# Performance work log

Measured on AMD Instinct MI355X. Metric: run time of the kernel, lower is better.

The kernel has to match this reference:

```python
import jax, jax.numpy as jnp
import numpy as np
from jax import lax

B, H, L, N, COUT = 16, 128, 8192, 16, 128
NEG_SLOPE = 0.3
BN_EPS = 1e-5


def setup_inputs() -> dict:
    key = jax.random.key(0)
    ks = jax.random.split(key, 20)
    x = jax.random.normal(ks[0], (B, H, L), dtype=jnp.float32)
    # --- S4D parameters ---
    log_dt = jnp.log(0.001) + jax.random.uniform(ks[1], (H,), dtype=jnp.float32) * (jnp.log(0.1) - jnp.log(0.001))
    A_log = jnp.log(0.5 * jnp.ones((H, N), dtype=jnp.float32))  # real part magnitude
    A_imag = jnp.broadcast_to(np.pi * jnp.arange(N, dtype=jnp.float32), (H, N)).copy()
    B_re = jnp.ones((H, N), dtype=jnp.float32)
    B_im = jnp.zeros((H, N), dtype=jnp.float32)
    C_re = jax.random.normal(ks[2], (H, N), dtype=jnp.float32) * (0.5 ** 0.5)
    C_im = jax.random.normal(ks[3], (H, N), dtype=jnp.float32) * (0.5 ** 0.5)
    D = jax.random.normal(ks[4], (H,), dtype=jnp.float32)
    # --- dilated conv branches (kernel_size=3, stride=4) ---
    wscale = 1.0 / np.sqrt(H * 3)
    w1 = jax.random.normal(ks[5], (COUT, H, 3), dtype=jnp.float32) * wscale
    b1 = jnp.zeros((COUT,), dtype=jnp.float32)
    w2 = jax.random.normal(ks[6], (COUT, H, 3), dtype=jnp.float32) * wscale
    b2 = jnp.zeros((COUT,), dtype=jnp.float32)
    w3 = jax.random.normal(ks[7], (COUT, H, 3), dtype=jnp.float32) * wscale
    b3 = jnp.zeros((COUT,), dtype=jnp.float32)
    w4 = jax.random.normal(ks[8], (COUT, H, 3), dtype=jnp.float32) * wscale
    b4 = jnp.zeros((COUT,), dtype=jnp.float32)
    gamma = jnp.ones((COUT,), dtype=jnp.float32)
    beta = jnp.zeros((COUT,), dtype=jnp.float32)
    return dict(x=x, log_dt=log_dt, A_log=A_log, A_imag=A_imag, B_re=B_re, B_im=B_im,
                C_re=C_re, C_im=C_im, D=D, w1=w1, b1=b1, w2=w2, b2=b2, w3=w3, b3=b3,
                w4=w4, b4=b4, gamma=gamma, beta=beta)


def _s4d(x, log_dt, A_log, A_imag, B_re, B_im, C_re, C_im, D):
    # x: (B,H,L). S4D with ZOH discretization, FFT long convolution.
    Lx = x.shape[-1]
    dt = jnp.exp(log_dt)[:, None]                    # (H,1)
    A = -jnp.exp(A_log) + 1j * A_imag                # (H,N)
    dtA = dt * A                                     # (H,N)
    dB = (jnp.exp(dtA) - 1.0) / A * (B_re + 1j * B_im)
    CB = (C_re + 1j * C_im) * dB                     # (H,N)
    l = jnp.arange(Lx, dtype=jnp.float32)
    vand = jnp.exp(dtA[:, :, None] * l)              # (H,N,L) Vandermonde
    K = 2.0 * jnp.real(jnp.einsum('hn,hnl->hl', CB, vand))  # (H,L)
    n = 2 * Lx
    Uf = jnp.fft.rfft(x, n=n)                        # (B,H,L+1)
    Kf = jnp.fft.rfft(K, n=n)                        # (H,L+1)
    y = jnp.fft.irfft(Uf * Kf, n=n)[..., :Lx]
    return y + D[:, None] * x


def _dconv(x, w, b, dil, pad):
    y = lax.conv_general_dilated(x, w, window_strides=(4,), padding=[(pad, pad)],
                                 rhs_dilation=(dil,), dimension_numbers=('NCH', 'OIH', 'NCH'))
    return y + b[:, None]


def _bn(z, gamma, beta):
    # training-mode BatchNorm1d: batch stats over (B, L_out) per channel
    m = jnp.mean(z, axis=(0, 2), keepdims=True)
    v = jnp.var(z, axis=(0, 2), keepdims=True)
    return gamma[:, None] * (z - m) * lax.rsqrt(v + BN_EPS) + beta[:, None]


def _lrelu(z):
    return jnp.where(z >= 0, z, NEG_SLOPE * z)


def reference(x, log_dt, A_log, A_imag, B_re, B_im, C_re, C_im, D,
              w1, b1, w2, b2, w3, b3, w4, b4, gamma, beta):
    y = _s4d(x, log_dt, A_log, A_imag, B_re, B_im, C_re, C_im, D)
    d1 = _bn(_dconv(y, w1, b1, 1, 1), gamma, beta)                 # no activation on branch 1
    d2 = _bn(_lrelu(_dconv(y, w2, b2, 2, 2)), gamma, beta)
    d3 = _bn(_lrelu(_dconv(y, w3, b3, 4, 4)), gamma, beta)
    d4 = _bn(_lrelu(_dconv(y, w4, b4, 8, 8)), gamma, beta)
    return jnp.concatenate([d1, d2, d3, d4], axis=1)               # (B, 4*COUT, L//4)
```

## Files before the change

kernel.cpp:

```cpp
#include <hip/hip_runtime.h>
#include <math.h>

typedef unsigned short u16x8 __attribute__((ext_vector_type(8)));
typedef unsigned short u16x2 __attribute__((ext_vector_type(2)));
typedef short s16x8 __attribute__((ext_vector_type(8)));
typedef float f32x4 __attribute__((ext_vector_type(4)));

__device__ __forceinline__ float bf2f(unsigned short u) {
    union { unsigned int i; float f; } v; v.i = ((unsigned int)u) << 16; return v.f;
}
__device__ __forceinline__ unsigned short f2bf(float f) {
    union { unsigned int i; float f; } v; v.f = f;
    unsigned int r = v.i + 0x7FFFu + ((v.i >> 16) & 1u);
    return (unsigned short)(r >> 16);
}

#define WB_OFF   163840
#define STAT_OFF 557056
#define Y_OFF    1048576
#define YT_OFF   34603008
#define Z_OFF    Y_OFF

__global__ void precompute_params(const float* __restrict__ log_dt,
                                  const float* __restrict__ A_log,
                                  const float* __restrict__ A_imag,
                                  const float* __restrict__ B_re,
                                  const float* __restrict__ B_im,
                                  const float* __restrict__ C_re,
                                  const float* __restrict__ C_im,
                                  float* __restrict__ params)
{
    int i = blockIdx.x * 256 + threadIdx.x;
    if (i >= 2048) return;
    int h = i >> 4;
    double dt = exp((double)log_dt[h]);
    double Ar = -exp((double)A_log[i]);
    double Ai = (double)A_imag[i];
    double dr = dt * Ar, di = dt * Ai;
    double ew = exp(dr);
    double wr = ew * cos(di), wi = ew * sin(di);
    double nr = wr - 1.0, ni = wi;
    double inv = 1.0 / (Ar * Ar + Ai * Ai);
    double tr = (nr * Ar + ni * Ai) * inv;
    double ti = (ni * Ar - nr * Ai) * inv;
    double Br = (double)B_re[i], Bi = (double)B_im[i];
    double dbr = tr * Br - ti * Bi, dbi = tr * Bi + ti * Br;
    double Cr = (double)C_re[i], Ci = (double)C_im[i];
    double cbr = Cr * dbr - Ci * dbi, cbi = Cr * dbi + Ci * dbr;
    params[i]        = (float)wr;
    params[2048 + i] = (float)wi;
    params[4096 + i] = (float)(2.0 * cbr);
    params[6144 + i] = (float)(2.0 * cbi);
    #pragma unroll
    for (int k = 0; k < 8; k++) {
        double mm = (double)(32 << k);
        double er = exp(mm * dr);
        params[8192 + k * 4096 + i]        = (float)(er * cos(mm * di));
        params[8192 + k * 4096 + 2048 + i] = (float)(er * sin(mm * di));
    }
}

__global__ void wpack(const float* __restrict__ w1, const float* __restrict__ w2,
                      const float* __restrict__ w3, const float* __restrict__ w4,
                      unsigned short* __restrict__ WB)
{
    int idx = blockIdx.x * 256 + threadIdx.x;
    int br = idx / 49152;
    int r  = idx - br * 49152;
    int co = r / 384;
    int k  = r - co * 384;
    int tap = k >> 7, h = k & 127;
    const float* wp = (br == 0) ? w1 : (br == 1) ? w2 : (br == 2) ? w3 : w4;
    WB[idx] = f2bf(wp[co * 384 + h * 3 + tap]);
}

__global__ __launch_bounds__(256, 2) void s4d_scan(const float* __restrict__ x,
                                                   const float* __restrict__ params,
                                                   const float* __restrict__ Dp,
                                                   unsigned short* __restrict__ yout)
{
    __shared__ float sbuf[256 * 33];
    __shared__ float spow[256];
    const int tid = threadIdx.x;
    const int bh = blockIdx.x;
    const int h = bh & 127;

    {
        int k = tid >> 5, r = tid & 31, n = r >> 1, c = r & 1;
        spow[tid] = params[8192 + k * 4096 + c * 2048 + (h << 4) + n];
    }

    float wre[16], wim[16];
    #pragma unroll
    for (int n = 0; n < 16; n++) {
        wre[n] = params[(h << 4) + n];
        wim[n] = params[2048 + (h << 4) + n];
    }

    const float4* xp4 = (const float4*)(x + (((size_t)bh) << 13) + (tid << 5));

    float zr[16], zi[16];
    #pragma unroll
    for (int n = 0; n < 16; n++) { zr[n] = 0.f; zi[n] = 0.f; }

    for (int s4v = 0; s4v < 8; s4v++) {
        float4 xv4 = xp4[s4v];
        #pragma unroll
        for (int e = 0; e < 4; e++) {
            float xv = (e == 0) ? xv4.x : (e == 1) ? xv4.y : (e == 2) ? xv4.z : xv4.w;
            #pragma unroll
            for (int n = 0; n < 16; n++) {
                float nr = fmaf(wre[n], zr[n], fmaf(-wim[n], zi[n], xv));
                float ni = fmaf(wim[n], zr[n], wre[n] * zi[n]);
                zr[n] = nr; zi[n] = ni;
            }
        }
    }
    __syncthreads();

    #pragma unroll 1
    for (int k = 0; k < 8; k++) {
        const int o = 1 << k;
        #pragma unroll
        for (int n = 0; n < 16; n++) {
            sbuf[tid * 33 + 2 * n]     = zr[n];
            sbuf[tid * 33 + 2 * n + 1] = zi[n];
        }
        __syncthreads();
        if (tid >= o) {
            const float* lp = &sbuf[(tid - o) * 33];
            #pragma unroll
            for (int n = 0; n < 16; n++) {
                float lr = lp[2 * n], li = lp[2 * n + 1];
                float mr = spow[(k << 5) + 2 * n], mi = spow[(k << 5) + 2 * n + 1];
                zr[n] = fmaf(mr, lr, fmaf(-mi, li, zr[n]));
                zi[n] = fmaf(mr, li, fmaf(mi, lr, zi[n]));
            }
        }
        __syncthreads();
    }

    #pragma unroll
    for (int n = 0; n < 16; n++) {
        sbuf[tid * 33 + 2 * n]     = zr[n];
        sbuf[tid * 33 + 2 * n + 1] = zi[n];
    }
    __syncthreads();
    if (tid == 0) {
        #pragma unroll
        for (int n = 0; n < 16; n++) { zr[n] = 0.f; zi[n] = 0.f; }
    } else {
        const float* lp = &sbuf[(tid - 1) * 33];
        #pragma unroll
        for (int n = 0; n < 16; n++) { zr[n] = lp[2 * n]; zi[n] = lp[2 * n + 1]; }
    }

    float cbr[16], cbi[16];
    #pragma unroll
    for (int n = 0; n < 16; n++) {
        cbr[n] = params[4096 + (h << 4) + n];
        cbi[n] = params[6144 + (h << 4) + n];
    }
    const float Dh = Dp[h];
    u16x8* yp8 = (u16x8*)(yout + (((size_t)bh) << 13) + (tid << 5));

    for (int s8 = 0; s8 < 4; s8++) {
        float4 xa = xp4[2 * s8], xb = xp4[2 * s8 + 1];
        u16x8 pk;
        #pragma unroll
        for (int e = 0; e < 8; e++) {
            float xv;
            switch (e) {
                case 0: xv = xa.x; break; case 1: xv = xa.y; break;
                case 2: xv = xa.z; break; case 3: xv = xa.w; break;
                case 4: xv = xb.x; break; case 5: xv = xb.y; break;
                case 6: xv = xb.z; break; default: xv = xb.w; break;
            }
            float acc = Dh * xv;
            #pragma unroll
            for (int n = 0; n < 16; n++) {
                float nr = fmaf(wre[n], zr[n], fmaf(-wim[n], zi[n], xv));
                float ni = fmaf(wim[n], zr[n], wre[n] * zi[n]);
                zr[n] = nr; zi[n] = ni;
                acc = fmaf(cbr[n], nr, fmaf(-cbi[n], ni, acc));
            }
            pk[e] = f2bf(acc);
        }
        yp8[s8] = pk;
    }
}

__global__ __launch_bounds__(256) void ytrans(const unsigned short* __restrict__ y,
                                              unsigned short* __restrict__ yT)
{
    __shared__ unsigned short sT[128 * 72];
    const int b = blockIdx.y, g0 = blockIdx.x << 6;
    const int tid = threadIdx.x;
    #pragma unroll
    for (int j = 0; j < 4; j++) {
        int li = tid + (j << 8);
        int h = li >> 3, g8 = (li & 7) << 3;
        u16x8 v = *(const u16x8*)(y + (((size_t)(b * 128 + h)) << 13) + g0 + g8);
        int gp = (g8 + (((h >> 3) & 7) << 3)) & 63;
        *(u16x8*)&sT[h * 72 + gp] = v;
    }
    __syncthreads();
    #pragma unroll
    for (int j = 0; j < 4; j++) {
        int li = tid + (j << 8);
        int g = li >> 4, h8 = (li & 15) << 3;
        u16x8 o;
        #pragma unroll
        for (int e = 0; e < 8; e++) {
            int h = h8 + e;
            int gp = (g + (((h >> 3) & 7) << 3)) & 63;
            o[e] = sT[h * 72 + gp];
        }
        *(u16x8*)(yT + (((size_t)(b * 8192 + g0 + g)) << 7) + h8) = o;
    }
}

__global__ __launch_bounds__(256) void conv_mfma(
    const unsigned short* __restrict__ yT,
    const unsigned short* __restrict__ WB,
    const float* __restrict__ b1, const float* __restrict__ b2,
    const float* __restrict__ b3, const float* __restrict__ b4,
    unsigned short* __restrict__ z)
{
    __shared__ unsigned short sW[128 * 40];
    __shared__ unsigned short sY[128 * 40];
    const int tid = threadIdx.x;
    const int lane = tid & 63, w = tid >> 6;
    const int branch = blockIdx.z, b = blockIdx.y;
    const int t0 = blockIdx.x << 7;
    const int d = 1 << branch;
    const int coH = (w & 1) << 6, tH = (w >> 1) << 6;
    const int ml = lane & 15, kg = lane >> 4;

    f32x4 acc[4][4];
    #pragma unroll
    for (int mt = 0; mt < 4; mt++)
        #pragma unroll
        for (int nt = 0; nt < 4; nt++) acc[mt][nt] = (f32x4)(0.f);

    const unsigned short* WBb = WB + (size_t)branch * 49152;

    for (int kc = 0; kc < 12; kc++) {
        const int tap = kc >> 2, hc = (kc & 3) << 5;
        const int goff = d * (tap - 1);
        __syncthreads();
        #pragma unroll
        for (int j = 0; j < 2; j++) {
            int li = tid + (j << 8);
            int co = li >> 2, kq = (li & 3) << 3;
            u16x8 v = *(const u16x8*)(WBb + (size_t)co * 384 + (kc << 5) + kq);
            *(u16x8*)&sW[co * 40 + kq] = v;
        }
        #pragma unroll
        for (int j = 0; j < 2; j++) {
            int li = tid + (j << 8);
            int n = li >> 2, kq = (li & 3) << 3;
            int g = ((t0 + n) << 2) + goff;
            u16x8 v;
            if ((unsigned)g < 8192u) {
                v = *(const u16x8*)(yT + (((size_t)(b * 8192 + g)) << 7) + hc + kq);
            } else {
                #pragma unroll
                for (int e = 0; e < 8; e++) v[e] = 0;
            }
            *(u16x8*)&sY[n * 40 + kq] = v;
        }
        __syncthreads();
        s16x8 af[4], bf[4];
        #pragma unroll
        for (int mt = 0; mt < 4; mt++)
            af[mt] = *(const s16x8*)&sW[(coH + mt * 16 + ml) * 40 + (kg << 3)];
        #pragma unroll
        for (int nt = 0; nt < 4; nt++)
            bf[nt] = *(const s16x8*)&sY[(tH + nt * 16 + ml) * 40 + (kg << 3)];
        #pragma unroll
        for (int mt = 0; mt < 4; mt++)
            #pragma unroll
            for (int nt = 0; nt < 4; nt++)
                acc[mt][nt] = __builtin_amdgcn_mfma_f32_16x16x32_bf16(af[mt], bf[nt], acc[mt][nt], 0, 0, 0);
    }

    const float* bp = (branch == 0) ? b1 : (branch == 1) ? b2 : (branch == 2) ? b3 : b4;
    #pragma unroll
    for (int mt = 0; mt < 4; mt++) {
        #pragma unroll
        for (int r = 0; r < 4; r++) {
            const int co = coH + mt * 16 + (kg << 2) + r;
            const float bb = bp[co];
            #pragma unroll
            for (int nt = 0; nt < 4; nt++) {
                const int t = t0 + tH + nt * 16 + ml;
                float v = acc[mt][nt][r] + bb;
                if (branch != 0) v = (v >= 0.f) ? v : 0.3f * v;
                z[(((size_t)((branch * 16 + b) * 128 + co)) << 11) + t] = f2bf(v);
            }
        }
    }
}

__global__ __launch_bounds__(256) void bn_stats(const unsigned short* __restrict__ z,
                                                float* __restrict__ stats)
{
    const int bc = blockIdx.x;
    const int branch = bc >> 7, co = bc & 127;
    const int tid = threadIdx.x;
    float s1 = 0.f, s2 = 0.f;
    for (int i = tid; i < 16384; i += 256) {
        int b = i >> 10, tp = (i & 1023) << 1;
        const unsigned short* p = z + (((size_t)((branch * 16 + b) * 128 + co)) << 11) + tp;
        u16x2 v2 = *(const u16x2*)p;
        float a = bf2f(v2[0]), c = bf2f(v2[1]);
        s1 += a + c;
        s2 = fmaf(a, a, fmaf(c, c, s2));
    }
    #pragma unroll
    for (int o = 32; o > 0; o >>= 1) { s1 += __shfl_down(s1, o); s2 += __shfl_down(s2, o); }
    __shared__ float r1[4], r2[4];
    const int lane = tid & 63, wid = tid >> 6;
    if (lane == 0) { r1[wid] = s1; r2[wid] = s2; }
    __syncthreads();
    if (tid == 0) {
        float t1 = r1[0] + r1[1] + r1[2] + r1[3];
        float t2 = r2[0] + r2[1] + r2[2] + r2[3];
        float m = t1 * (1.0f / 32768.0f);
        float var = t2 * (1.0f / 32768.0f) - m * m;
        stats[bc * 2]     = m;
        stats[bc * 2 + 1] = 1.0f / sqrtf(var + 1e-5f);
    }
}

__global__ __launch_bounds__(256) void bn_apply(const unsigned short* __restrict__ z,
                                                const float* __restrict__ stats,
                                                const float* __restrict__ gam,
                                                const float* __restrict__ bet,
                                                float* __restrict__ out)
{
    const size_t idx = (((size_t)blockIdx.x << 8) + threadIdx.x) << 3;
    const int t = (int)(idx & 2047);
    const size_t bc = idx >> 11;
    const int ch = (int)(bc & 511);
    const int b = (int)(bc >> 9);
    const int branch = ch >> 7, co = ch & 127;
    const float m = stats[ch * 2], inv = stats[ch * 2 + 1];
    const float ga = gam[co], be = bet[co];
    const float sc = ga * inv, sh = fmaf(-m, sc, be);
    const unsigned short* zp = z + (((size_t)((branch * 16 + b) * 128 + co)) << 11) + t;
    u16x8 v = *(const u16x8*)zp;
    float4 o0, o1;
    o0.x = fmaf(bf2f(v[0]), sc, sh); o0.y = fmaf(bf2f(v[1]), sc, sh);
    o0.z = fmaf(bf2f(v[2]), sc, sh); o0.w = fmaf(bf2f(v[3]), sc, sh);
    o1.x = fmaf(bf2f(v[4]), sc, sh); o1.y = fmaf(bf2f(v[5]), sc, sh);
    o1.z = fmaf(bf2f(v[6]), sc, sh); o1.w = fmaf(bf2f(v[7]), sc, sh);
    *(float4*)(out + idx)     = o0;
    *(float4*)(out + idx + 4) = o1;
}

extern "C" void kernel_launch(void* const* d_in, const int* in_sizes, int n_in,
                              void* d_out, int out_size, void* d_ws, size_t ws_size,
                              hipStream_t stream) {
    const float* x      = (const float*)d_in[0];
    const float* log_dt = (const float*)d_in[1];
    const float* A_log  = (const float*)d_in[2];
    const float* A_imag = (const float*)d_in[3];
    const float* B_re   = (const float*)d_in[4];
    const float* B_im   = (const float*)d_in[5];
    const float* C_re   = (const float*)d_in[6];
    const float* C_im   = (const float*)d_in[7];
    const float* Dp     = (const float*)d_in[8];
    const float* w1 = (const float*)d_in[9];
    const float* b1 = (const float*)d_in[10];
    const float* w2 = (const float*)d_in[11];
    const float* b2 = (const float*)d_in[12];
    const float* w3 = (const float*)d_in[13];
    const float* b3 = (const float*)d_in[14];
    const float* w4 = (const float*)d_in[15];
    const float* b4 = (const float*)d_in[16];
    const float* gam = (const float*)d_in[17];
    const float* bet = (const float*)d_in[18];

    float* params = (float*)d_ws;
    unsigned short* WBp = (unsigned short*)((char*)d_ws + WB_OFF);
    float* stats = (float*)((char*)d_ws + STAT_OFF);
    unsigned short* yws = (unsigned short*)((char*)d_ws + Y_OFF);
    unsigned short* yT  = (unsigned short*)((char*)d_ws + YT_OFF);
    unsigned short* zws = (unsigned short*)((char*)d_ws + Z_OFF);
    float* out = (float*)d_out;

    precompute_params<<<dim3(8), dim3(256), 0, stream>>>(log_dt, A_log, A_imag,
                                                         B_re, B_im, C_re, C_im, params);
    wpack<<<dim3(768), dim3(256), 0, stream>>>(w1, w2, w3, w4, WBp);
    s4d_scan<<<dim3(2048), dim3(256), 0, stream>>>(x, params, Dp, yws);
    ytrans<<<dim3(128, 16), dim3(256), 0, stream>>>(yws, yT);
    conv_mfma<<<dim3(16, 16, 4), dim3(256), 0, stream>>>(yT, WBp, b1, b2, b3, b4, zws);
    bn_stats<<<dim3(512), dim3(256), 0, stream>>>(zws, stats);
    bn_apply<<<dim3(8192), dim3(256), 0, stream>>>(zws, stats, gam, bet, out);
}
```

Measured before the change: 294.9 us.

## Replace sequential S4D chunk recurrence with bf16 MFMA chunked state-space matmuls

After: 284.1 us. 3.7% less time.

```diff
diff --git a/kernel.cpp b/kernel.cpp
--- a/kernel.cpp
+++ b/kernel.cpp
@@ -15,48 +15,96 @@
     return (unsigned short)(r >> 16);
 }
 
-#define WB_OFF   163840
-#define STAT_OFF 557056
+#define MATS_OFF 16384
+#define WB_OFF   548864
+#define STAT_OFF 942080
 #define Y_OFF    1048576
 #define YT_OFF   34603008
 #define Z_OFF    Y_OFF
 
-__global__ void precompute_params(const float* __restrict__ log_dt,
-                                  const float* __restrict__ A_log,
-                                  const float* __restrict__ A_imag,
-                                  const float* __restrict__ B_re,
-                                  const float* __restrict__ B_im,
-                                  const float* __restrict__ C_re,
-                                  const float* __restrict__ C_im,
-                                  float* __restrict__ params)
-{
-    int i = blockIdx.x * 256 + threadIdx.x;
-    if (i >= 2048) return;
-    int h = i >> 4;
-    double dt = exp((double)log_dt[h]);
-    double Ar = -exp((double)A_log[i]);
-    double Ai = (double)A_imag[i];
-    double dr = dt * Ar, di = dt * Ai;
-    double ew = exp(dr);
-    double wr = ew * cos(di), wi = ew * sin(di);
-    double nr = wr - 1.0, ni = wi;
-    double inv = 1.0 / (Ar * Ar + Ai * Ai);
-    double tr = (nr * Ar + ni * Ai) * inv;
-    double ti = (ni * Ar - nr * Ai) * inv;
-    double Br = (double)B_re[i], Bi = (double)B_im[i];
-    double dbr = tr * Br - ti * Bi, dbi = tr * Bi + ti * Br;
-    double Cr = (double)C_re[i], Ci = (double)C_im[i];
-    double cbr = Cr * dbr - Ci * dbi, cbi = Cr * dbi + Ci * dbr;
-    params[i]        = (float)wr;
-    params[2048 + i] = (float)wi;
-    params[4096 + i] = (float)(2.0 * cbr);
-    params[6144 + i] = (float)(2.0 * cbi);
-    #pragma unroll
-    for (int k = 0; k < 8; k++) {
-        double mm = (double)(32 << k);
-        double er = exp(mm * dr);
-        params[8192 + k * 4096 + i]        = (float)(er * cos(mm * di));
-        params[8192 + k * 4096 + 2048 + i] = (float)(er * sin(mm * di));
+__global__ void precompute_s4d(const float* __restrict__ log_dt,
+                               const float* __restrict__ A_log,
+                               const float* __restrict__ A_imag,
+                               const float* __restrict__ B_re,
+                               const float* __restrict__ B_im,
+                               const float* __restrict__ C_re,
+                               const float* __restrict__ C_im,
+                               float* __restrict__ w32,
+                               unsigned short* __restrict__ MATS)
+{
+    const int h = blockIdx.x;
+    const int tid = threadIdx.x;
+    const double dt = exp((double)log_dt[h]);
+
+    #pragma unroll 1
+    for (int it = 0; it < 4; it++) {
+        int idx = tid + (it << 8);
+        int s = idx >> 5, i = idx & 31;
+        int n = s >> 1;
+        double Ar = -exp((double)A_log[h * 16 + n]);
+        double Ai = (double)A_imag[h * 16 + n];
+        double dr = dt * Ar, di = dt * Ai;
+        double l = (double)(31 - i);
+        double e = exp(l * dr);
+        double val = (s & 1) ? e * sin(l * di) : e * cos(l * di);
+        MATS[(size_t)h * 2080 + s * 32 + i] = f2bf((float)val);
+    }
+    #pragma unroll 1
+    for (int it = 0; it < 4; it++) {
+        int idx = tid + (it << 8);
+        int j = idx >> 5, s = idx & 31;
+        int n = s >> 1;
+        double Ar = -exp((double)A_log[h * 16 + n]);
+        double Ai = (double)A_imag[h * 16 + n];
+        double dr = dt * Ar, di = dt * Ai;
+        double ew = exp(dr);
+        double wr = ew * cos(di), wi = ew * sin(di);
+        double nr = wr - 1.0, ni = wi;
+        double inv = 1.0 / (Ar * Ar + Ai * Ai);
+        double tr = (nr * Ar + ni * Ai) * inv;
+        double ti = (ni * Ar - nr * Ai) * inv;
+        double Br = (double)B_re[h * 16 + n], Bi = (double)B_im[h * 16 + n];
+        double dbr = tr * Br - ti * Bi, dbi = tr * Bi + ti * Br;
+        double Cr = (double)C_re[h * 16 + n], Ci = (double)C_im[h * 16 + n];
+        double cbr = Cr * dbr - Ci * dbi, cbi = Cr * dbi + Ci * dbr;
+        double m = (double)(j + 1);
+        double e = exp(m * dr);
+        double pr = e * cos(m * di), pi = e * sin(m * di);
+        double gr = cbr * pr - cbi * pi, gi = cbr * pi + cbi * pr;
+        double val = (s & 1) ? -2.0 * gi : 2.0 * gr;
+        MATS[(size_t)h * 2080 + 1024 + j * 32 + s] = f2bf((float)val);
+    }
+    if (tid < 32) {
+        double l = (double)tid;
+        double acc = 0.0;
+        for (int n = 0; n < 16; n++) {
+            double Ar = -exp((double)A_log[h * 16 + n]);
+            double Ai = (double)A_imag[h * 16 + n];
+            double dr = dt * Ar, di = dt * Ai;
+            double ew = exp(dr);
+            double wr = ew * cos(di), wi = ew * sin(di);
+            double nr = wr - 1.0, ni = wi;
+            double inv = 1.0 / (Ar * Ar + Ai * Ai);
+            double tr = (nr * Ar + ni * Ai) * inv;
+            double ti = (ni * Ar - nr * Ai) * inv;
+            double Br = (double)B_re[h * 16 + n], Bi = (double)B_im[h * 16 + n];
+            double dbr = tr * Br - ti * Bi, dbi = tr * Bi + ti * Br;
+            double Cr = (double)C_re[h * 16 + n], Ci = (double)C_im[h * 16 + n];
+            double cbr = Cr * dbr - Ci * dbi, cbi = Cr * dbi + Ci * dbr;
+            double e = exp(l * dr);
+            double wlr = e * cos(l * di), wli = e * sin(l * di);
+            acc += cbr * wlr - cbi * wli;
+        }
+        MATS[(size_t)h * 2080 + 2048 + tid] = f2bf((float)(2.0 * acc));
+    }
+    if (tid < 16) {
+        int n = tid;
+        double Ar = -exp((double)A_log[h * 16 + n]);
+        double Ai = (double)A_imag[h * 16 + n];
+        double dr = dt * Ar, di = dt * Ai;
+        double e = exp(32.0 * dr);
+        w32[h * 32 + 2 * n]     = (float)(e * cos(32.0 * di));
+        w32[h * 32 + 2 * n + 1] = (float)(e * sin(32.0 * di));
     }
 }
 
@@ -74,47 +122,96 @@
     WB[idx] = f2bf(wp[co * 384 + h * 3 + tap]);
 }
 
-__global__ __launch_bounds__(256, 2) void s4d_scan(const float* __restrict__ x,
-                                                   const float* __restrict__ params,
+__global__ __launch_bounds__(256, 2) void s4d_mfma(const float* __restrict__ x,
+                                                   const float* __restrict__ w32,
+                                                   const unsigned short* __restrict__ MATS,
                                                    const float* __restrict__ Dp,
                                                    unsigned short* __restrict__ yout)
 {
-    __shared__ float sbuf[256 * 33];
-    __shared__ float spow[256];
+    __shared__ unsigned short sXc[256 * 40];
+    __shared__ unsigned short sM[3840];
+    __shared__ float spow2[256];
+    __shared__ unsigned short skr[32];
+    __shared__ float scratch[8448];
     const int tid = threadIdx.x;
     const int bh = blockIdx.x;
     const int h = bh & 127;
-
+    const int lane = tid & 63, w = tid >> 6;
+    const int ml = lane & 15, kg = lane >> 4;
+
+    float xr[32];
+    const float4* xp4 = (const float4*)(x + ((size_t)bh << 13) + (tid << 5));
+    #pragma unroll
+    for (int i = 0; i < 8; i++) {
+        float4 v = xp4[i];
+        xr[4 * i] = v.x; xr[4 * i + 1] = v.y; xr[4 * i + 2] = v.z; xr[4 * i + 3] = v.w;
+    }
+    #pragma unroll
+    for (int g = 0; g < 4; g++) {
+        u16x8 pk;
+        #pragma unroll
+        for (int e = 0; e < 8; e++) pk[e] = f2bf(xr[g * 8 + e]);
+        *(u16x8*)&sXc[tid * 40 + g * 8] = pk;
+    }
     {
-        int k = tid >> 5, r = tid & 31, n = r >> 1, c = r & 1;
-        spow[tid] = params[8192 + k * 4096 + c * 2048 + (h << 4) + n];
-    }
-
-    float wre[16], wim[16];
+        int matv = tid >> 7, r = (tid >> 2) & 31, sg = tid & 3;
+        u16x8 v = *(const u16x8*)(MATS + (size_t)h * 2080 + matv * 1024 + r * 32 + sg * 8);
+        *(u16x8*)&sM[matv * 2560 + r * 40 + sg * 8] = v;
+    }
+    if (tid < 4) {
+        u16x8 v = *(const u16x8*)(MATS + (size_t)h * 2080 + 2048 + tid * 8);
+        *(u16x8*)&skr[tid * 8] = v;
+    }
+    if (tid < 16) {
+        float rr = w32[h * 32 + 2 * tid], ii = w32[h * 32 + 2 * tid + 1];
+        #pragma unroll
+        for (int k = 0; k < 8; k++) {
+            spow2[k * 32 + 2 * tid] = rr; spow2[k * 32 + 2 * tid + 1] = ii;
+            float n2r = rr * rr - ii * ii, n2i = 2.f * rr * ii;
+            rr = n2r; ii = n2i;
+        }
+    }
+    __syncthreads();
+    #pragma unroll
+    for (int it = 0; it < 4; it++) {
+        int idx = tid + (it << 8);
+        int j = idx >> 5, i = idx & 31;
+        sM[1280 + j * 40 + i] = (i <= j) ? skr[j - i] : (unsigned short)0;
+    }
+    __syncthreads();
+
+    f32x4 acc[2][4];
+    #pragma unroll
+    for (int mt = 0; mt < 2; mt++)
+        #pragma unroll
+        for (int nt = 0; nt < 4; nt++) acc[mt][nt] = (f32x4)(0.f);
+    {
+        s16x8 af[2], bfr[4];
+        #pragma unroll
+        for (int mt = 0; mt < 2; mt++)
+            af[mt] = *(const s16x8*)&sM[(mt * 16 + ml) * 40 + kg * 8];
+        #pragma unroll
+        for (int nt = 0; nt < 4; nt++)
+            bfr[nt] = *(const s16x8*)&sXc[(w * 64 + nt * 16 + ml) * 40 + kg * 8];
+        #pragma unroll
+        for (int mt = 0; mt < 2; mt++)
+            #pragma unroll
+            for (int nt = 0; nt < 4; nt++)
+                acc[mt][nt] = __builtin_amdgcn_mfma_f32_16x16x32_bf16(af[mt], bfr[nt], acc[mt][nt], 0, 0, 0);
+    }
+    #pragma unroll
+    for (int mt = 0; mt < 2; mt++)
+        #pragma unroll
+        for (int nt = 0; nt < 4; nt++)
+            #pragma unroll
+            for (int r = 0; r < 4; r++)
+                scratch[(mt * 16 + kg * 4 + r) * 264 + (w * 64 + nt * 16 + ml)] = acc[mt][nt][r];
+    __syncthreads();
+    float zr[16], zi[16];
     #pragma unroll
     for (int n = 0; n < 16; n++) {
-        wre[n] = params[(h << 4) + n];
-        wim[n] = params[2048 + (h << 4) + n];
-    }
-
-    const float4* xp4 = (const float4*)(x + (((size_t)bh) << 13) + (tid << 5));
-
-    float zr[16], zi[16];
-    #pragma unroll
-    for (int n = 0; n < 16; n++) { zr[n] = 0.f; zi[n] = 0.f; }
-
-    for (int s4v = 0; s4v < 8; s4v++) {
-        float4 xv4 = xp4[s4v];
-        #pragma unroll
-        for (int e = 0; e < 4; e++) {
-            float xv = (e == 0) ? xv4.x : (e == 1) ? xv4.y : (e == 2) ? xv4.z : xv4.w;
-            #pragma unroll
-            for (int n = 0; n < 16; n++) {
-                float nr = fmaf(wre[n], zr[n], fmaf(-wim[n], zi[n], xv));
-                float ni = fmaf(wim[n], zr[n], wre[n] * zi[n]);
-                zr[n] = nr; zi[n] = ni;
-            }
-        }
+        zr[n] = scratch[(2 * n) * 264 + tid];
+        zi[n] = scratch[(2 * n + 1) * 264 + tid];
     }
     __syncthreads();
 
@@ -123,70 +220,97 @@
         const int o = 1 << k;
         #pragma unroll
         for (int n = 0; n < 16; n++) {
-            sbuf[tid * 33 + 2 * n]     = zr[n];
-            sbuf[tid * 33 + 2 * n + 1] = zi[n];
+            scratch[tid * 33 + 2 * n]     = zr[n];
+            scratch[tid * 33 + 2 * n + 1] = zi[n];
         }
         __syncthreads();
         if (tid >= o) {
-            const float* lp = &sbuf[(tid - o) * 33];
+            const float* lp = &scratch[(tid - o) * 33];
             #pragma unroll
             for (int n = 0; n < 16; n++) {
                 float lr = lp[2 * n], li = lp[2 * n + 1];
-                float mr = spow[(k << 5) + 2 * n], mi = spow[(k << 5) + 2 * n + 1];
+                float mr = spow2[(k << 5) + 2 * n], mi = spow2[(k << 5) + 2 * n + 1];
                 zr[n] = fmaf(mr, lr, fmaf(-mi, li, zr[n]));
                 zi[n] = fmaf(mr, li, fmaf(mi, lr, zi[n]));
             }
         }
         __syncthreads();
     }
-
     #pragma unroll
     for (int n = 0; n < 16; n++) {
-        sbuf[tid * 33 + 2 * n]     = zr[n];
-        sbuf[tid * 33 + 2 * n + 1] = zi[n];
+        scratch[tid * 33 + 2 * n]     = zr[n];
+        scratch[tid * 33 + 2 * n + 1] = zi[n];
     }
     __syncthreads();
     if (tid == 0) {
         #pragma unroll
         for (int n = 0; n < 16; n++) { zr[n] = 0.f; zi[n] = 0.f; }
     } else {
-        const float* lp = &sbuf[(tid - 1) * 33];
+        const float* lp = &scratch[(tid - 1) * 33];
         #pragma unroll
         for (int n = 0; n < 16; n++) { zr[n] = lp[2 * n]; zi[n] = lp[2 * n + 1]; }
     }
-
-    float cbr[16], cbi[16];
-    #pragma unroll
-    for (int n = 0; n < 16; n++) {
-        cbr[n] = params[4096 + (h << 4) + n];
-        cbi[n] = params[6144 + (h << 4) + n];
-    }
+    __syncthreads();
+    {
+        unsigned short* sCc = (unsigned short*)scratch;
+        #pragma unroll
+        for (int g = 0; g < 4; g++) {
+            u16x8 pk;
+            #pragma unroll
+            for (int q = 0; q < 4; q++) {
+                pk[2 * q]     = f2bf(zr[g * 4 + q]);
+                pk[2 * q + 1] = f2bf(zi[g * 4 + q]);
+            }
+            *(u16x8*)&sCc[tid * 40 + g * 8] = pk;
+        }
+    }
+    __syncthreads();
+
+    #pragma unroll
+    for (int mt = 0; mt < 2; mt++)
+        #pragma unroll
+        for (int nt = 0; nt < 4; nt++) acc[mt][nt] = (f32x4)(0.f);
+    {
+        const unsigned short* sCc = (const unsigned short*)scratch;
+        s16x8 a1[2], a2[2], bfx[4], bfc[4];
+        #pragma unroll
+        for (int mt = 0; mt < 2; mt++) {
+            a1[mt] = *(const s16x8*)&sM[1280 + (mt * 16 + ml) * 40 + kg * 8];
+            a2[mt] = *(const s16x8*)&sM[2560 + (mt * 16 + ml) * 40 + kg * 8];
+        }
+        #pragma unroll
+        for (int nt = 0; nt < 4; nt++) {
+            bfx[nt] = *(const s16x8*)&sXc[(w * 64 + nt * 16 + ml) * 40 + kg * 8];
+            bfc[nt] = *(const s16x8*)&sCc[(w * 64 + nt * 16 + ml) * 40 + kg * 8];
+        }
+        #pragma unroll
+        for (int mt = 0; mt < 2; mt++)
+            #pragma unroll
+            for (int nt = 0; nt < 4; nt++) {
+                acc[mt][nt] = __builtin_amdgcn_mfma_f32_16x16x32_bf16(a1[mt], bfx[nt], acc[mt][nt], 0, 0, 0);
+                acc[mt][nt] = __builtin_amdgcn_mfma_f32_16x16x32_bf16(a2[mt], bfc[nt], acc[mt][nt], 0, 0, 0);
+            }
+    }
+    __syncthreads();
+    #pragma unroll
+    for (int mt = 0; mt < 2; mt++)
+        #pragma unroll
+        for (int nt = 0; nt < 4; nt++)
+            #pragma unroll
+            for (int r = 0; r < 4; r++)
+                scratch[(mt * 16 + kg * 4 + r) * 264 + (w * 64 + nt * 16 + ml)] = acc[mt][nt][r];
+    __syncthreads();
     const float Dh = Dp[h];
-    u16x8* yp8 = (u16x8*)(yout + (((size_t)bh) << 13) + (tid << 5));
-
-    for (int s8 = 0; s8 < 4; s8++) {
-        float4 xa = xp4[2 * s8], xb = xp4[2 * s8 + 1];
+    u16x8* yp = (u16x8*)(yout + ((size_t)bh << 13) + (tid << 5));
+    #pragma unroll
+    for (int g = 0; g < 4; g++) {
         u16x8 pk;
         #pragma unroll
         for (int e = 0; e < 8; e++) {
-            float xv;
-            switch (e) {
-                case 0: xv = xa.x; break; case 1: xv = xa.y; break;
-                case 2: xv = xa.z; break; case 3: xv = xa.w; break;
-                case 4: xv = xb.x; break; case 5: xv = xb.y; break;
-                case 6: xv = xb.z; break; default: xv = xb.w; break;
-            }
-            float acc = Dh * xv;
-            #pragma unroll
-            for (int n = 0; n < 16; n++) {
-                float nr = fmaf(wre[n], zr[n], fmaf(-wim[n], zi[n], xv));
-                float ni = fmaf(wim[n], zr[n], wre[n] * zi[n]);
-                zr[n] = nr; zi[n] = ni;
-                acc = fmaf(cbr[n], nr, fmaf(-cbi[n], ni, acc));
-            }
-            pk[e] = f2bf(acc);
-        }
-        yp8[s8] = pk;
+            int i = g * 8 + e;
+            pk[e] = f2bf(fmaf(Dh, xr[i], scratch[i * 264 + tid]));
+        }
+        yp[g] = pk;
     }
 }
 
@@ -271,18 +395,18 @@
             *(u16x8*)&sY[n * 40 + kq] = v;
         }
         __syncthreads();
-        s16x8 af[4], bf[4];
+        s16x8 af[4], bfr[4];
         #pragma unroll
         for (int mt = 0; mt < 4; mt++)
             af[mt] = *(const s16x8*)&sW[(coH + mt * 16 + ml) * 40 + (kg << 3)];
         #pragma unroll
         for (int nt = 0; nt < 4; nt++)
-            bf[nt] = *(const s16x8*)&sY[(tH + nt * 16 + ml) * 40 + (kg << 3)];
+            bfr[nt] = *(const s16x8*)&sY[(tH + nt * 16 + ml) * 40 + (kg << 3)];
         #pragma unroll
         for (int mt = 0; mt < 4; mt++)
             #pragma unroll
             for (int nt = 0; nt < 4; nt++)
-                acc[mt][nt] = __builtin_amdgcn_mfma_f32_16x16x32_bf16(af[mt], bf[nt], acc[mt][nt], 0, 0, 0);
+                acc[mt][nt] = __builtin_amdgcn_mfma_f32_16x16x32_bf16(af[mt], bfr[nt], acc[mt][nt], 0, 0, 0);
     }
 
     const float* bp = (branch == 0) ? b1 : (branch == 1) ? b2 : (branch == 2) ? b3 : b4;
@@ -383,7 +507,8 @@
     const float* gam = (const float*)d_in[17];
     const float* bet = (const float*)d_in[18];
 
-    float* params = (float*)d_ws;
+    float* w32p = (float*)d_ws;
+    unsigned short* MATSp = (unsigned short*)((char*)d_ws + MATS_OFF);
     unsigned short* WBp = (unsigned short*)((char*)d_ws + WB_OFF);
     float* stats = (float*)((char*)d_ws + STAT_OFF);
     unsigned short* yws = (unsigned short*)((char*)d_ws + Y_OFF);
@@ -391,10 +516,10 @@
     unsigned short* zws = (unsigned short*)((char*)d_ws + Z_OFF);
     float* out = (float*)d_out;
 
-    precompute_params<<<dim3(8), dim3(256), 0, stream>>>(log_dt, A_log, A_imag,
-                                                         B_re, B_im, C_re, C_im, params);
+    precompute_s4d<<<dim3(128), dim3(256), 0, stream>>>(log_dt, A_log, A_imag,
+                                                        B_re, B_im, C_re, C_im, w32p, MATSp);
     wpack<<<dim3(768), dim3(256), 0, stream>>>(w1, w2, w3, w4, WBp);
-    s4d_scan<<<dim3(2048), dim3(256), 0, stream>>>(x, params, Dp, yws);
+    s4d_mfma<<<dim3(2048), dim3(256), 0, stream>>>(x, w32p, MATSp, Dp, yws);
     ytrans<<<dim3(128, 16), dim3(256), 0, stream>>>(yws, yT);
     conv_mfma<<<dim3(16, 16, 4), dim3(256), 0, stream>>>(yT, WBp, b1, b2, b3, b4, zws);
     bn_stats<<<dim3(512), dim3(256), 0, stream>>>(zws, stats);
```
